# Performance work log

Measured on AMD Instinct MI355X. Metric: run time of the kernel, lower is better.

## Reference

```python
import jax, jax.numpy as jnp
import numpy as np

THETA = 10000.0

def _rope(t):
    # lucidrains-style interleaved rotary over the FULL last dim (dim=hidden_size)
    T, d = t.shape[-2], t.shape[-1]
    freqs = 1.0 / (THETA ** (jnp.arange(0, d, 2, dtype=jnp.float32) / d))  # (d/2,)
    ang = jnp.arange(T, dtype=jnp.float32)[:, None] * freqs[None, :]       # (T, d/2)
    ang = jnp.repeat(ang, 2, axis=-1)                                      # (T, d) interleaved
    cos, sin = jnp.cos(ang), jnp.sin(ang)
    x = t.reshape(t.shape[:-1] + (d // 2, 2))
    x1, x2 = x[..., 0], x[..., 1]
    rot = jnp.stack([-x2, x1], axis=-1).reshape(t.shape)  # rotate_half, interleaved pairs
    return t * cos + rot * sin


def setup_inputs() -> dict:
    key = jax.random.key(0)
    ks = jax.random.split(key, 5)
    B, T, C = 4, 2048, 1024
    s = 0.02
    return {
        "x":  jax.random.normal(ks[0], (B, T, C), dtype=jnp.float32),
        "Wq": jax.random.normal(ks[1], (C, C), dtype=jnp.float32) * s,
        "bq": jnp.zeros((C,), dtype=jnp.float32),
        "Wk": jax.random.normal(ks[2], (C, C), dtype=jnp.float32) * s,
        "bk": jnp.zeros((C,), dtype=jnp.float32),
        "Wv": jax.random.normal(ks[3], (C, C), dtype=jnp.float32) * s,
        "bv": jnp.zeros((C,), dtype=jnp.float32),
        "Wf": jax.random.normal(ks[4], (C, C), dtype=jnp.float32) * s,
        "bf": jnp.zeros((C,), dtype=jnp.float32),
    }


def reference(x, Wq, bq, Wk, bk, Wv, bv, Wf, bf):
    B, T, C = x.shape
    Q = _rope(x @ Wq.T + bq)
    K = _rope(x @ Wk.T + bk)
    V = x @ Wv.T + bv
    # scores [B,T,T]; _get_D(gamma=1, T) is exactly a causal lower-triangular mask
    A = jnp.einsum('btd,bsd->bts', Q, K) / jnp.sqrt(jnp.float32(C))
    causal = jnp.tril(jnp.ones((T, T), dtype=bool))
    A = jnp.where(causal, A, -jnp.inf)
    A = jax.nn.softmax(A, axis=-1)
    out = jnp.einsum('bts,bsd->btd', A, V)
    return out @ Wf.T + bf
```

## Files before the change

### kernel.cpp

```cpp
#include <hip/hip_runtime.h>
#include <math.h>


#define AS1(p) ((__attribute__((address_space(1))) void*)(p))
#define AS3(p) ((__attribute__((address_space(3))) void*)(p))

typedef __attribute__((ext_vector_type(8))) short bf16x8;
typedef __attribute__((ext_vector_type(4))) float f32x4;

__device__ __forceinline__ unsigned short f2bf(float f) {
  unsigned int u = __float_as_uint(f);
  u += 0x7fffu + ((u >> 16) & 1u);
  return (unsigned short)(u >> 16);
}

__global__ __launch_bounds__(256) void cast_all(
    const float* __restrict__ x, const float* __restrict__ Wq,
    const float* __restrict__ Wk, const float* __restrict__ Wv,
    const float* __restrict__ Wf,
    unsigned short* __restrict__ xb, unsigned short* __restrict__ Wqb,
    unsigned short* __restrict__ Wkb, unsigned short* __restrict__ Wvb,
    unsigned short* __restrict__ Wfb) {
  int i = blockIdx.x * 256 + threadIdx.x;
  const float* src; unsigned short* dst; int off;
  if (i < 2097152) { src = x; dst = xb; off = i; }
  else {
    int j = i - 2097152;
    int w = j >> 18; off = j & 262143;
    src = (w == 0) ? Wq : (w == 1) ? Wk : (w == 2) ? Wv : Wf;
    dst = (w == 0) ? Wqb : (w == 1) ? Wkb : (w == 2) ? Wvb : Wfb;
  }
  float4 f = ((const float4*)src)[off];
  ushort4 o;
  o.x = f2bf(f.x); o.y = f2bf(f.y); o.z = f2bf(f.z); o.w = f2bf(f.w);
  ((ushort4*)dst)[off] = o;
}

__device__ __forceinline__ void gemm_core(const unsigned short* __restrict__ At, long long lda,
                                          const unsigned short* __restrict__ Bt, long long ldb,
                                          int K, f32x4 (&acc)[4][4],
                                          unsigned short* As, unsigned short* Bs) {
  const int tid  = threadIdx.x;
  const int lane = tid & 63;
  const int w    = tid >> 6;
  const int wm   = (w & 1) << 6;
  const int wn   = (w >> 1) << 6;
  const int fr   = lane & 15;
  const int fq   = lane >> 4;
  const int srow = tid >> 2;
  const int scol = (tid & 3) << 3;
  const int lg   = ((tid & 3) ^ ((srow >> 1) & 3)) << 3;
  const unsigned short* a0 = At + (long long)srow * lda + lg;
  const unsigned short* a1 = At + (long long)(srow + 64) * lda + lg;
  const unsigned short* b0 = Bt + (long long)srow * ldb + lg;
  const unsigned short* b1 = Bt + (long long)(srow + 64) * ldb + lg;
  unsigned short* As0 = As + srow * 32 + scol;
  unsigned short* As1 = As + (srow + 64) * 32 + scol;
  unsigned short* Bs0 = Bs + srow * 32 + scol;
  unsigned short* Bs1 = Bs + (srow + 64) * 32 + scol;
  const int pg = (fq ^ ((fr >> 1) & 3)) << 3;
  for (int k0 = 0; k0 < K; k0 += 32) {
    __builtin_amdgcn_global_load_lds(AS1(a0 + k0), AS3(As0), 16, 0, 0);
    __builtin_amdgcn_global_load_lds(AS1(a1 + k0), AS3(As1), 16, 0, 0);
    __builtin_amdgcn_global_load_lds(AS1(b0 + k0), AS3(Bs0), 16, 0, 0);
    __builtin_amdgcn_global_load_lds(AS1(b1 + k0), AS3(Bs1), 16, 0, 0);
    __syncthreads();
    bf16x8 af[4], bfr[4];
#pragma unroll
    for (int i = 0; i < 4; i++)
      af[i] = *(const bf16x8*)(As + (wm + i * 16 + fr) * 32 + pg);
#pragma unroll
    for (int i = 0; i < 4; i++)
      bfr[i] = *(const bf16x8*)(Bs + (wn + i * 16 + fr) * 32 + pg);
#pragma unroll
    for (int mi = 0; mi < 4; mi++)
#pragma unroll
      for (int ni = 0; ni < 4; ni++)
        acc[mi][ni] = __builtin_amdgcn_mfma_f32_16x16x32_bf16(af[mi], bfr[ni], acc[mi][ni], 0, 0, 0);
    __syncthreads();
  }
}

__device__ __forceinline__ void repack_store_mi(unsigned short (&vals)[4][4],
                                                unsigned short* sh, int mi,
                                                int m0, int n0, long long ldo,
                                                unsigned short* __restrict__ Out) {
  const int tid = threadIdx.x, lane = tid & 63, w = tid >> 6;
  const int half = w & 1, wn = (w >> 1) << 6;
  const int cl = lane & 15, q4 = lane >> 4;
  const int lr = half * 16 + q4 * 4;
#pragma unroll
  for (int ni = 0; ni < 4; ni++)
#pragma unroll
    for (int rr = 0; rr < 4; rr++)
      sh[(lr + rr) * 132 + wn + ni * 16 + cl] = vals[ni][rr];
  __syncthreads();
#pragma unroll
  for (int it = 0; it < 2; ++it) {
    int row = (tid >> 4) + it * 16;
    int c8 = (tid & 15) << 3;
    bf16x8 v = *(const bf16x8*)(sh + row * 132 + c8);
    int gr = m0 + (row < 16 ? mi * 16 + row : 48 + mi * 16 + row);
    *(bf16x8*)(Out + (long long)gr * ldo + n0 + c8) = v;
  }
  __syncthreads();
}

__global__ __launch_bounds__(256) void proj_rope(
    const unsigned short* __restrict__ xb,
    const unsigned short* __restrict__ Wq, const unsigned short* __restrict__ Wk,
    const unsigned short* __restrict__ Wv,
    const float* __restrict__ bq, const float* __restrict__ bk, const float* __restrict__ bv,
    unsigned short* __restrict__ Q, unsigned short* __restrict__ Ko,
    unsigned short* __restrict__ V) {
  __shared__ unsigned short sh[8192];
  const int m0 = blockIdx.x * 128;
  const int n0 = blockIdx.y * 128;
  const int which = blockIdx.z;
  const unsigned short* W = which == 0 ? Wq : (which == 1 ? Wk : Wv);
  const float* bias = which == 0 ? bq : (which == 1 ? bk : bv);
  unsigned short* Out = which == 0 ? Q : (which == 1 ? Ko : V);
  const bool rope = which < 2;

  f32x4 acc[4][4];
#pragma unroll
  for (int i = 0; i < 4; i++)
#pragma unroll
    for (int j = 0; j < 4; j++)
#pragma unroll
      for (int k = 0; k < 4; k++) acc[i][j][k] = 0.0f;

  gemm_core(xb + (long long)m0 * 1024, 1024, W + (long long)n0 * 1024, 1024, 1024, acc, sh, sh + 4096);

  const int tid = threadIdx.x, lane = tid & 63, w = tid >> 6;
  const int wm = (w & 1) << 6, wn = (w >> 1) << 6;
  const int cl = lane & 15, q4 = lane >> 4;
  const float NEG_L2T_512 = -0.025952563239354392f;
  const float INV2PI = 0.15915494309189535f;
  float freqn[4];
#pragma unroll
  for (int ni = 0; ni < 4; ni++) {
    int gn = n0 + wn + ni * 16 + cl;
    freqn[ni] = exp2f(NEG_L2T_512 * (float)(gn >> 1));
  }
#pragma unroll
  for (int mi = 0; mi < 4; mi++) {
    unsigned short vals[4][4];
    const int t0 = (m0 & 2047) + wm + mi * 16 + q4 * 4;
#pragma unroll
    for (int ni = 0; ni < 4; ni++) {
      const int gn = n0 + wn + ni * 16 + cl;
#pragma unroll
      for (int rr = 0; rr < 4; rr++) {
        float v = acc[mi][ni][rr] + bias[gn];
        if (rope) {
          float partner = __shfl_xor(v, 1, 64);
          float ang = (float)(t0 + rr) * freqn[ni];
          float rev = ang * INV2PI;
          rev = rev - floorf(rev);
          float c = __builtin_amdgcn_cosf(rev);
          float s = __builtin_amdgcn_sinf(rev);
          v = v * c + ((gn & 1) ? partner : -partner) * s;
        }
        vals[ni][rr] = f2bf(v);
      }
    }
    repack_store_mi(vals, sh, mi, m0, n0, 1024, Out);
  }
}

__global__ __launch_bounds__(256) void transpose_v(const unsigned short* __restrict__ V,
                                                   unsigned short* __restrict__ Vt) {
  __shared__ unsigned short tle[64][65];
  const int b = blockIdx.z;
  const int s0 = blockIdx.x * 64, d0 = blockIdx.y * 64;
  const unsigned short* Vb = V + (long long)b * 2048 * 1024;
  unsigned short* Tb = Vt + (long long)b * 1024 * 2048;
  const int tid = threadIdx.x;
  union U { uint4 v; unsigned short u[8]; };
#pragma unroll
  for (int it = 0; it < 2; ++it) {
    int idx = tid + it * 256;
    int r = idx >> 3, c8 = (idx & 7) << 3;
    U d;
    d.v = *(const uint4*)(Vb + (long long)(s0 + r) * 1024 + d0 + c8);
#pragma unroll
    for (int j = 0; j < 8; j++) tle[r][c8 + j] = d.u[j];
  }
  __syncthreads();
#pragma unroll
  for (int it = 0; it < 2; ++it) {
    int idx = tid + it * 256;
    int r = idx >> 3, c8 = (idx & 7) << 3;
    U o;
#pragma unroll
    for (int j = 0; j < 8; j++) o.u[j] = tle[c8 + j][r];
    *(uint4*)(Tb + (long long)(d0 + r) * 2048 + s0 + c8) = o.v;
  }
}

__global__ __launch_bounds__(256) void score_exp(const unsigned short* __restrict__ Q,
                                                 const unsigned short* __restrict__ Kk,
                                                 unsigned short* __restrict__ P,
                                                 float* __restrict__ row_sum) {
  if (blockIdx.y > blockIdx.x) return;
  __shared__ unsigned short sh[8192];
  const int b = blockIdx.z;
  const int m0 = blockIdx.x * 128, n0 = blockIdx.y * 128;
  const unsigned short* Qb = Q + (long long)b * 2048 * 1024;
  const unsigned short* Kb = Kk + (long long)b * 2048 * 1024;
  unsigned short* Pb = P + (long long)b * 2048 * 2048;
  float* rs = row_sum + b * 2048;

  f32x4 acc[4][4];
#pragma unroll
  for (int i = 0; i < 4; i++)
#pragma unroll
    for (int j = 0; j < 4; j++)
#pragma unroll
      for (int k = 0; k < 4; k++) acc[i][j][k] = 0.0f;

  gemm_core(Qb + (long long)m0 * 1024, 1024, Kb + (long long)n0 * 1024, 1024, 1024, acc, sh, sh + 4096);

  const int tid = threadIdx.x, lane = tid & 63, w = tid >> 6;
  const int wm = (w & 1) << 6, wn = (w >> 1) << 6;
  const int cl = lane & 15, q4 = lane >> 4;
  const bool diag = (blockIdx.x == blockIdx.y);
#pragma unroll
  for (int mi = 0; mi < 4; mi++) {
    unsigned short vals[4][4];
    float rsum[4] = {0.f, 0.f, 0.f, 0.f};
#pragma unroll
    for (int ni = 0; ni < 4; ni++) {
      const int gn = n0 + wn + ni * 16 + cl;
#pragma unroll
      for (int rr = 0; rr < 4; rr++) {
        const int gm = m0 + wm + mi * 16 + q4 * 4 + rr;
        float e = (diag && gn > gm) ? 0.0f : __expf(acc[mi][ni][rr] * 0.03125f);
        vals[ni][rr] = f2bf(e);
        rsum[rr] += e;
      }
    }
#pragma unroll
    for (int rr = 0; rr < 4; rr++) {
#pragma unroll
      for (int off = 1; off < 16; off <<= 1) rsum[rr] += __shfl_xor(rsum[rr], off, 64);
    }
    if (cl == 0) {
      const int gm = m0 + wm + mi * 16 + q4 * 4;
#pragma unroll
      for (int rr = 0; rr < 4; rr++) atomicAdd(&rs[gm + rr], rsum[rr]);
    }
    repack_store_mi(vals, sh, mi, m0, n0, 2048, Pb);
  }
}

__global__ __launch_bounds__(256) void pv_gemm(const unsigned short* __restrict__ P,
                                               const unsigned short* __restrict__ Vt,
                                               const float* __restrict__ row_sum,
                                               unsigned short* __restrict__ O) {
  __shared__ unsigned short sh[8192];
  const int b = blockIdx.z;
  const int m0 = blockIdx.x * 128;
  const int n0 = blockIdx.y * 128;
  const unsigned short* Pb = P + (long long)b * 2048 * 2048;
  const unsigned short* Vb = Vt + (long long)b * 1024 * 2048;
  const float* rs = row_sum + b * 2048;
  const int K = m0 + 128;

  f32x4 acc[4][4];
#pragma unroll
  for (int i = 0; i < 4; i++)
#pragma unroll
    for (int j = 0; j < 4; j++)
#pragma unroll
      for (int k = 0; k < 4; k++) acc[i][j][k] = 0.0f;

  gemm_core(Pb + (long long)m0 * 2048, 2048, Vb + (long long)n0 * 2048, 2048, K, acc, sh, sh + 4096);

  const int tid = threadIdx.x, lane = tid & 63, w = tid >> 6;
  const int wm = (w & 1) << 6;
  const int q4 = lane >> 4;
#pragma unroll
  for (int mi = 0; mi < 4; mi++) {
    unsigned short vals[4][4];
    float inv[4];
    const int gm0 = m0 + wm + mi * 16 + q4 * 4;
#pragma unroll
    for (int rr = 0; rr < 4; rr++) inv[rr] = 1.0f / rs[gm0 + rr];
#pragma unroll
    for (int ni = 0; ni < 4; ni++)
#pragma unroll
      for (int rr = 0; rr < 4; rr++)
        vals[ni][rr] = f2bf(acc[mi][ni][rr] * inv[rr]);
    repack_store_mi(vals, sh, mi, m0, n0, 1024, O + (long long)b * 2048 * 1024);
  }
}

__global__ __launch_bounds__(256) void final_gemm(const unsigned short* __restrict__ O,
                                                  const unsigned short* __restrict__ Wf,
                                                  const float* __restrict__ bf_,
                                                  float* __restrict__ out) {
  __shared__ unsigned short sh[8448];
  float* shf = (float*)sh;
  const int m0 = blockIdx.x * 128;
  const int n0 = blockIdx.y * 128;

  f32x4 acc[4][4];
#pragma unroll
  for (int i = 0; i < 4; i++)
#pragma unroll
    for (int j = 0; j < 4; j++)
#pragma unroll
      for (int k = 0; k < 4; k++) acc[i][j][k] = 0.0f;

  gemm_core(O + (long long)m0 * 1024, 1024, Wf + (long long)n0 * 1024, 1024, 1024, acc, sh, sh + 4096);

  const int tid = threadIdx.x, lane = tid & 63, w = tid >> 6;
  const int half = w & 1, wn = (w >> 1) << 6;
  const int cl = lane & 15, q4 = lane >> 4;
  const int lr = half * 16 + q4 * 4;
#pragma unroll
  for (int mi = 0; mi < 4; mi++) {
#pragma unroll
    for (int ni = 0; ni < 4; ni++)
#pragma unroll
      for (int rr = 0; rr < 4; rr++)
        shf[(lr + rr) * 130 + wn + ni * 16 + cl] = acc[mi][ni][rr] + bf_[n0 + wn + ni * 16 + cl];
    __syncthreads();
    {
      int row = tid >> 3;
      int c4 = (tid & 7) << 4;
      int gr = m0 + (row < 16 ? mi * 16 + row : 48 + mi * 16 + row);
      float* dst = out + (long long)gr * 1024 + n0 + c4;
      const float* srcp = shf + row * 130 + c4;
#pragma unroll
      for (int j = 0; j < 4; j++)
        ((float4*)dst)[j] = ((const float4*)srcp)[j];
    }
    __syncthreads();
  }
}

extern "C" void kernel_launch(void* const* d_in, const int* in_sizes, int n_in,
                              void* d_out, int out_size, void* d_ws, size_t ws_size,
                              hipStream_t stream) {
  (void)in_sizes; (void)n_in; (void)out_size; (void)ws_size;
  const float* x   = (const float*)d_in[0];
  const float* Wq  = (const float*)d_in[1];
  const float* bq  = (const float*)d_in[2];
  const float* Wk  = (const float*)d_in[3];
  const float* bk  = (const float*)d_in[4];
  const float* Wv  = (const float*)d_in[5];
  const float* bv  = (const float*)d_in[6];
  const float* Wf  = (const float*)d_in[7];
  const float* bf_ = (const float*)d_in[8];
  float* out = (float*)d_out;

  char* ws = (char*)d_ws;
  const size_t MB = 1024 * 1024;
  unsigned short* xb  = (unsigned short*)(ws);
  unsigned short* Wqb = (unsigned short*)(ws + 16 * MB);
  unsigned short* Wkb = (unsigned short*)(ws + 18 * MB);
  unsigned short* Wvb = (unsigned short*)(ws + 20 * MB);
  unsigned short* Wfb = (unsigned short*)(ws + 22 * MB);
  unsigned short* Qb  = (unsigned short*)(ws + 24 * MB);
  unsigned short* Kb  = (unsigned short*)(ws + 40 * MB);
  unsigned short* Vtb = (unsigned short*)(ws + 56 * MB);
  unsigned short* Ob  = (unsigned short*)(ws + 72 * MB);
  unsigned short* Vb  = (unsigned short*)(ws + 88 * MB);
  unsigned short* Pb  = (unsigned short*)(ws + 88 * MB);
  float*          rsum= (float*)(ws + 120 * MB);

  dim3 blk(256);
  hipMemsetAsync(rsum, 0, 8192 * sizeof(float), stream);
  cast_all<<<dim3(3145728 / 256), blk, 0, stream>>>(x, Wq, Wk, Wv, Wf, xb, Wqb, Wkb, Wvb, Wfb);
  proj_rope<<<dim3(64, 8, 3), blk, 0, stream>>>(xb, Wqb, Wkb, Wvb, bq, bk, bv, Qb, Kb, Vb);
  transpose_v<<<dim3(32, 16, 4), blk, 0, stream>>>(Vb, Vtb);
  score_exp<<<dim3(16, 16, 4), blk, 0, stream>>>(Qb, Kb, Pb, rsum);
  pv_gemm<<<dim3(16, 8, 4), blk, 0, stream>>>(Pb, Vtb, rsum, Ob);
  final_gemm<<<dim3(64, 8), blk, 0, stream>>>(Ob, Wfb, bf_, out);
}
```

Measured before the change: 320.7 us.

## Fuse V transpose into projection epilogue, compact causal grid, reverse PV tile order

The V projection epilogue now writes its tile transposed through shared memory straight into Vt, which removes the separate transpose kernel and its extra 16MB read and write round trip. The score kernel launches only the 136 lower-triangular tiles per batch and decodes each tile index with a sqrt-based mapping, so no blocks are launched only to exit early. The PV GEMM schedules the longest-K row tiles first to balance the causal workload. Shared memory in proj_rope grows to about 34KB, which may reduce occupancy.

Result: faster. 310.3 us (-3.2%).

```diff
diff --git a/kernel.cpp b/kernel.cpp
--- a/kernel.cpp
+++ b/kernel.cpp
@@ -112,14 +112,13 @@
     const unsigned short* __restrict__ Wv,
     const float* __restrict__ bq, const float* __restrict__ bk, const float* __restrict__ bv,
     unsigned short* __restrict__ Q, unsigned short* __restrict__ Ko,
-    unsigned short* __restrict__ V) {
-  __shared__ unsigned short sh[8192];
+    unsigned short* __restrict__ Vt) {
+  __shared__ unsigned short sh[17408];
   const int m0 = blockIdx.x * 128;
   const int n0 = blockIdx.y * 128;
   const int which = blockIdx.z;
   const unsigned short* W = which == 0 ? Wq : (which == 1 ? Wk : Wv);
   const float* bias = which == 0 ? bq : (which == 1 ? bk : bv);
-  unsigned short* Out = which == 0 ? Q : (which == 1 ? Ko : V);
   const bool rope = which < 2;
 
   f32x4 acc[4][4];
@@ -135,6 +134,39 @@
   const int tid = threadIdx.x, lane = tid & 63, w = tid >> 6;
   const int wm = (w & 1) << 6, wn = (w >> 1) << 6;
   const int cl = lane & 15, q4 = lane >> 4;
+
+  if (which == 2) {
+#pragma unroll
+    for (int mi = 0; mi < 4; mi++)
+#pragma unroll
+      for (int ni = 0; ni < 4; ni++) {
+        const int d = wn + ni * 16 + cl;
+        const float b_ = bias[n0 + d];
+#pragma unroll
+        for (int rr = 0; rr < 4; rr++) {
+          const int tr = wm + mi * 16 + q4 * 4 + rr;
+          sh[d * 136 + tr] = f2bf(acc[mi][ni][rr] + b_);
+        }
+      }
+    __syncthreads();
+    const int b = m0 >> 11;
+    const int sloc = m0 & 2047;
+    unsigned short* Vb = Vt + (long long)b * 1024 * 2048;
+#pragma unroll
+    for (int it = 0; it < 4; ++it) {
+      int ci = tid + it * 256;
+      int r = ci >> 3;
+      int c16 = (ci & 7) << 4;
+      bf16x8 v0 = *(const bf16x8*)(sh + r * 136 + c16);
+      bf16x8 v1 = *(const bf16x8*)(sh + r * 136 + c16 + 8);
+      unsigned short* dst = Vb + (long long)(n0 + r) * 2048 + sloc + c16;
+      *(bf16x8*)dst = v0;
+      *(bf16x8*)(dst + 8) = v1;
+    }
+    return;
+  }
+
+  unsigned short* Out = which == 0 ? Q : Ko;
   const float NEG_L2T_512 = -0.025952563239354392f;
   const float INV2PI = 0.15915494309189535f;
   float freqn[4];
@@ -153,49 +185,17 @@
 #pragma unroll
       for (int rr = 0; rr < 4; rr++) {
         float v = acc[mi][ni][rr] + bias[gn];
-        if (rope) {
-          float partner = __shfl_xor(v, 1, 64);
-          float ang = (float)(t0 + rr) * freqn[ni];
-          float rev = ang * INV2PI;
-          rev = rev - floorf(rev);
-          float c = __builtin_amdgcn_cosf(rev);
-          float s = __builtin_amdgcn_sinf(rev);
-          v = v * c + ((gn & 1) ? partner : -partner) * s;
-        }
+        float partner = __shfl_xor(v, 1, 64);
+        float ang = (float)(t0 + rr) * freqn[ni];
+        float rev = ang * INV2PI;
+        rev = rev - floorf(rev);
+        float c = __builtin_amdgcn_cosf(rev);
+        float s = __builtin_amdgcn_sinf(rev);
+        v = v * c + ((gn & 1) ? partner : -partner) * s;
         vals[ni][rr] = f2bf(v);
       }
     }
     repack_store_mi(vals, sh, mi, m0, n0, 1024, Out);
-  }
-}
-
-__global__ __launch_bounds__(256) void transpose_v(const unsigned short* __restrict__ V,
-                                                   unsigned short* __restrict__ Vt) {
-  __shared__ unsigned short tle[64][65];
-  const int b = blockIdx.z;
-  const int s0 = blockIdx.x * 64, d0 = blockIdx.y * 64;
-  const unsigned short* Vb = V + (long long)b * 2048 * 1024;
-  unsigned short* Tb = Vt + (long long)b * 1024 * 2048;
-  const int tid = threadIdx.x;
-  union U { uint4 v; unsigned short u[8]; };
-#pragma unroll
-  for (int it = 0; it < 2; ++it) {
-    int idx = tid + it * 256;
-    int r = idx >> 3, c8 = (idx & 7) << 3;
-    U d;
-    d.v = *(const uint4*)(Vb + (long long)(s0 + r) * 1024 + d0 + c8);
-#pragma unroll
-    for (int j = 0; j < 8; j++) tle[r][c8 + j] = d.u[j];
-  }
-  __syncthreads();
-#pragma unroll
-  for (int it = 0; it < 2; ++it) {
-    int idx = tid + it * 256;
-    int r = idx >> 3, c8 = (idx & 7) << 3;
-    U o;
-#pragma unroll
-    for (int j = 0; j < 8; j++) o.u[j] = tle[c8 + j][r];
-    *(uint4*)(Tb + (long long)(d0 + r) * 2048 + s0 + c8) = o.v;
   }
 }
 
@@ -203,10 +203,14 @@
                                                  const unsigned short* __restrict__ Kk,
                                                  unsigned short* __restrict__ P,
                                                  float* __restrict__ row_sum) {
-  if (blockIdx.y > blockIdx.x) return;
   __shared__ unsigned short sh[8192];
+  const int bx = blockIdx.x;
+  int i = (int)((sqrtf(8.0f * (float)bx + 1.0f) - 1.0f) * 0.5f);
+  while ((i + 1) * (i + 2) / 2 <= bx) ++i;
+  while (i * (i + 1) / 2 > bx) --i;
+  const int j = bx - i * (i + 1) / 2;
   const int b = blockIdx.z;
-  const int m0 = blockIdx.x * 128, n0 = blockIdx.y * 128;
+  const int m0 = i * 128, n0 = j * 128;
   const unsigned short* Qb = Q + (long long)b * 2048 * 1024;
   const unsigned short* Kb = Kk + (long long)b * 2048 * 1024;
   unsigned short* Pb = P + (long long)b * 2048 * 2048;
@@ -214,18 +218,18 @@
 
   f32x4 acc[4][4];
 #pragma unroll
-  for (int i = 0; i < 4; i++)
-#pragma unroll
-    for (int j = 0; j < 4; j++)
-#pragma unroll
-      for (int k = 0; k < 4; k++) acc[i][j][k] = 0.0f;
+  for (int ii = 0; ii < 4; ii++)
+#pragma unroll
+    for (int jj = 0; jj < 4; jj++)
+#pragma unroll
+      for (int k = 0; k < 4; k++) acc[ii][jj][k] = 0.0f;
 
   gemm_core(Qb + (long long)m0 * 1024, 1024, Kb + (long long)n0 * 1024, 1024, 1024, acc, sh, sh + 4096);
 
   const int tid = threadIdx.x, lane = tid & 63, w = tid >> 6;
   const int wm = (w & 1) << 6, wn = (w >> 1) << 6;
   const int cl = lane & 15, q4 = lane >> 4;
-  const bool diag = (blockIdx.x == blockIdx.y);
+  const bool diag = (i == j);
 #pragma unroll
   for (int mi = 0; mi < 4; mi++) {
     unsigned short vals[4][4];
@@ -261,7 +265,8 @@
                                                unsigned short* __restrict__ O) {
   __shared__ unsigned short sh[8192];
   const int b = blockIdx.z;
-  const int m0 = blockIdx.x * 128;
+  const int mt = 15 - blockIdx.x;
+  const int m0 = mt * 128;
   const int n0 = blockIdx.y * 128;
   const unsigned short* Pb = P + (long long)b * 2048 * 2048;
   const unsigned short* Vb = Vt + (long long)b * 1024 * 2048;
@@ -368,16 +373,14 @@
   unsigned short* Kb  = (unsigned short*)(ws + 40 * MB);
   unsigned short* Vtb = (unsigned short*)(ws + 56 * MB);
   unsigned short* Ob  = (unsigned short*)(ws + 72 * MB);
-  unsigned short* Vb  = (unsigned short*)(ws + 88 * MB);
   unsigned short* Pb  = (unsigned short*)(ws + 88 * MB);
   float*          rsum= (float*)(ws + 120 * MB);
 
   dim3 blk(256);
   hipMemsetAsync(rsum, 0, 8192 * sizeof(float), stream);
   cast_all<<<dim3(3145728 / 256), blk, 0, stream>>>(x, Wq, Wk, Wv, Wf, xb, Wqb, Wkb, Wvb, Wfb);
-  proj_rope<<<dim3(64, 8, 3), blk, 0, stream>>>(xb, Wqb, Wkb, Wvb, bq, bk, bv, Qb, Kb, Vb);
-  transpose_v<<<dim3(32, 16, 4), blk, 0, stream>>>(Vb, Vtb);
-  score_exp<<<dim3(16, 16, 4), blk, 0, stream>>>(Qb, Kb, Pb, rsum);
+  proj_rope<<<dim3(64, 8, 3), blk, 0, stream>>>(xb, Wqb, Wkb, Wvb, bq, bk, bv, Qb, Kb, Vtb);
+  score_exp<<<dim3(136, 1, 4), blk, 0, stream>>>(Qb, Kb, Pb, rsum);
   pv_gemm<<<dim3(16, 8, 4), blk, 0, stream>>>(Pb, Vtb, rsum, Ob);
   final_gemm<<<dim3(64, 8), blk, 0, stream>>>(Ob, Wfb, bf_, out);
 }
```
